# Kernel optimization log

Measured on AMD Instinct MI355X. Metric: run time of the kernel, lower is better.

The kernel has to match this reference:

```python
import jax, jax.numpy as jnp
import numpy as np

B = 64; SEQ = 512; PRED = 96; D = 321; HID = 2048
WIN = 64; STRIDE = WIN // 2; FT = WIN // 2 + 1
LOW = int(FT * 0.3); MID = int(FT * 0.4); HIGH = FT - LOW - MID  # 9, 13, 11
NW = SEQ // STRIDE + 1; EMBED = NW * WIN  # 17, 1088
EPS = 1e-5; SCALE = 0.02
LH = int(LOW * 2.0); MH = int(MID * 2.0); HH = int(HIGH * 2.0)  # 18, 26, 22


def _clayer(key, fan_in, fan_out):
    k1, k2, k3, k4 = jax.random.split(key, 4)
    return (jax.random.normal(k1, (fan_in, fan_out), jnp.float32) * SCALE,
            jax.random.normal(k2, (fan_in, fan_out), jnp.float32) * SCALE,
            jax.random.normal(k3, (fan_out,), jnp.float32) * SCALE,
            jax.random.normal(k4, (fan_out,), jnp.float32) * SCALE)


def setup_inputs() -> dict:
    key = jax.random.key(0)
    ks = jax.random.split(key, 12)
    inp = {}
    inp["x"] = jax.random.normal(ks[0], (B, SEQ, D), jnp.float32)
    inp["x_mark_enc"] = jax.random.normal(ks[1], (B, SEQ, 4), jnp.float32)
    inp["x_dec"] = jax.random.normal(ks[2], (B, PRED, D), jnp.float32)
    inp["x_mark_dec"] = jax.random.normal(ks[3], (B, PRED, 4), jnp.float32)
    n = jnp.arange(WIN, dtype=jnp.float32)
    inp["window"] = 0.5 * (1.0 - jnp.cos(2.0 * jnp.pi * n / WIN))  # torch.hann_window (periodic)
    inp["revin_w"] = jnp.ones((D,), jnp.float32)
    inp["revin_b"] = jnp.zeros((D,), jnp.float32)
    # low band filter: 3 complex layers LOW->LH->LH->LOW
    for i, (fi, fo) in enumerate([(LOW, LH), (LH, LH), (LH, LOW)]):
        wr, wi, br, bi = _clayer(jax.random.fold_in(ks[4], i), fi, fo)
        inp[f"low{i}_wr"], inp[f"low{i}_wi"], inp[f"low{i}_br"], inp[f"low{i}_bi"] = wr, wi, br, bi
    # mid band filter: 2 complex layers MID->MH->MID
    for i, (fi, fo) in enumerate([(MID, MH), (MH, MID)]):
        wr, wi, br, bi = _clayer(jax.random.fold_in(ks[5], i), fi, fo)
        inp[f"mid{i}_wr"], inp[f"mid{i}_wi"], inp[f"mid{i}_br"], inp[f"mid{i}_bi"] = wr, wi, br, bi
    # high band filter: 1 complex layer HIGH->HIGH
    wr, wi, br, bi = _clayer(ks[6], HIGH, HIGH)
    inp["high0_wr"], inp["high0_wi"], inp["high0_br"], inp["high0_bi"] = wr, wi, br, bi
    inp["fc1_w"] = jax.random.normal(ks[7], (EMBED, HID), jnp.float32) * SCALE
    inp["fc1_b"] = jnp.zeros((HID,), jnp.float32)
    inp["fc2_w"] = jax.random.normal(ks[8], (HID, PRED), jnp.float32) * SCALE
    inp["fc2_b"] = jnp.zeros((PRED,), jnp.float32)
    return inp


def _clin(z, wr, wi, br, bi):
    return z @ (wr + 1j * wi) + (br + 1j * bi)


def _cact(z):
    return jax.nn.leaky_relu(z.real) + 1j * jax.nn.leaky_relu(z.imag)


def reference(x, x_mark_enc, x_dec, x_mark_dec, window, revin_w, revin_b,
              low0_wr, low0_wi, low0_br, low0_bi,
              low1_wr, low1_wi, low1_br, low1_bi,
              low2_wr, low2_wi, low2_br, low2_bi,
              mid0_wr, mid0_wi, mid0_br, mid0_bi,
              mid1_wr, mid1_wi, mid1_br, mid1_bi,
              high0_wr, high0_wi, high0_br, high0_bi,
              fc1_w, fc1_b, fc2_w, fc2_b):
    # RevIN norm over time dim
    mean = jnp.mean(x, axis=1, keepdims=True)
    std = jnp.sqrt(jnp.var(x, axis=1, keepdims=True) + EPS)
    xn = (x - mean) / std * revin_w + revin_b
    xc = jnp.transpose(xn, (0, 2, 1))                      # [B, D, L]
    xp = jnp.pad(xc, ((0, 0), (0, 0), (STRIDE, STRIDE)))
    # batched window extraction (replaces python loop over windows)
    idx = jnp.arange(NW)[:, None] * STRIDE + jnp.arange(WIN)[None, :]
    seg = xp[:, :, idx]
    w = window / jnp.linalg.norm(window)
    xf = jnp.fft.rfft(seg * w, axis=-1)                    # [B, D, NW, FT] complex
    low = xf[..., :LOW]
    mid = xf[..., LOW:LOW + MID]
    high = xf[..., LOW + MID:]
    low = _clin(_cact(_clin(_cact(_clin(low, low0_wr, low0_wi, low0_br, low0_bi)),
                            low1_wr, low1_wi, low1_br, low1_bi)),
                low2_wr, low2_wi, low2_br, low2_bi)
    mid = _clin(_cact(_clin(mid, mid0_wr, mid0_wi, mid0_br, mid0_bi)),
                mid1_wr, mid1_wi, mid1_br, mid1_bi)
    high = _clin(high, high0_wr, high0_wi, high0_br, high0_bi)
    xfil = jnp.concatenate([low, mid, high], axis=-1)      # [B, D, NW, FT]
    xt = jnp.fft.irfft(xfil, n=WIN, axis=-1)
    emb = xt.reshape(x.shape[0], D, EMBED)
    h = jax.nn.leaky_relu(emb @ fc1_w + fc1_b)
    y = h @ fc2_w + fc2_b                                  # [B, D, PRED]
    y = jnp.transpose(y, (0, 2, 1))                        # [B, PRED, D]
    # RevIN denorm
    y = (y - revin_b) / (revin_w + EPS * EPS) * std + mean
    return y
```

## Files before the change

### kernel.cpp

```cpp
#include <hip/hip_runtime.h>

typedef unsigned short u16;
typedef unsigned int   u32;
typedef __attribute__((ext_vector_type(4))) float  fvec4;
typedef __attribute__((ext_vector_type(8))) __bf16 bvec8;

#define NB    64
#define SEQL  512
#define DCH   321
#define BDTOT (NB * DCH)
#define NWIN  17
#define PREDL 96
#define MWTOT (BDTOT * NWIN)
#define KPAD  1152

__device__ __forceinline__ u16 f2bf(float f) {
    union { float f; u32 u; } v; v.f = f;
    u32 r = v.u + 0x7FFFu + ((v.u >> 16) & 1u);
    return (u16)(r >> 16);
}
__device__ __forceinline__ float lrelu(float v) { return v > 0.f ? v : 0.01f * v; }

__device__ __forceinline__ void gld16(const u16* g, u16* l) {
    __builtin_amdgcn_global_load_lds((const __attribute__((address_space(1))) void*)g,
                                     (__attribute__((address_space(3))) void*)l, 16, 0, 0);
}

__global__ __launch_bounds__(256) void stats_kernel(const float* __restrict__ x,
                                                    float* __restrict__ mean,
                                                    float* __restrict__ rstd,
                                                    float* __restrict__ stdv) {
    __shared__ float ls[2][4][64];
    int i = threadIdx.x & 63;
    int j = threadIdx.x >> 6;
    int bd = blockIdx.x * 64 + i;
    int b = bd / DCH, d = bd - b * DCH;
    float s = 0.f, ss = 0.f;
    for (int t = j; t < SEQL; t += 4) {
        float v = x[((size_t)b * SEQL + t) * DCH + d];
        s += v; ss += v * v;
    }
    ls[0][j][i] = s; ls[1][j][i] = ss;
    __syncthreads();
    if (j == 0) {
        s  = ls[0][0][i] + ls[0][1][i] + ls[0][2][i] + ls[0][3][i];
        ss = ls[1][0][i] + ls[1][1][i] + ls[1][2][i] + ls[1][3][i];
        float m   = s * (1.f / SEQL);
        float var = ss * (1.f / SEQL) - m * m;
        float st  = sqrtf(var + 1e-5f);
        mean[bd] = m; rstd[bd] = 1.f / st; stdv[bd] = st;
    }
}

__global__ __launch_bounds__(256) void norm_transpose(const float* __restrict__ x,
                                                      const float* __restrict__ mean,
                                                      const float* __restrict__ rstd,
                                                      const float* __restrict__ rw,
                                                      const float* __restrict__ rb,
                                                      u16* __restrict__ xnT) {
    __shared__ float tile[64][65];
    int d0 = blockIdx.x * 64, s0 = blockIdx.y * 64, b = blockIdx.z;
    for (int e = threadIdx.x; e < 4096; e += 256) {
        int sr = e >> 6, dc = e & 63;
        int d = d0 + dc;
        tile[sr][dc] = (d < DCH) ? x[((size_t)b * SEQL + s0 + sr) * DCH + d] : 0.f;
    }
    __syncthreads();
    for (int e = threadIdx.x; e < 4096; e += 256) {
        int dr = e >> 6, sc = e & 63;
        int d = d0 + dr;
        if (d < DCH) {
            int bd = b * DCH + d;
            float v = (tile[sc][dr] - mean[bd]) * rstd[bd] * rw[d] + rb[d];
            xnT[(size_t)bd * 576 + 32 + s0 + sc] = f2bf(v);
        }
    }
}

__global__ __launch_bounds__(256) void pad_zero(u16* __restrict__ xnT) {
    int idx = blockIdx.x * 256 + threadIdx.x;
    if (idx < BDTOT * 64) {
        int bd = idx >> 6, q = idx & 63;
        int off = q < 32 ? q : 512 + q;
        xnT[(size_t)bd * 576 + off] = 0;
    }
}

__global__ __launch_bounds__(256) void pad_emb(u16* __restrict__ EMB) {
    int idx = blockIdx.x * 256 + threadIdx.x;
    if (idx < BDTOT * 8) {
        int bd = idx >> 3, o = (idx & 7) * 8;
        fvec4 z = {0.f, 0.f, 0.f, 0.f};
        *(fvec4*)&EMB[(size_t)bd * KPAD + 1088 + o] = z;
    }
}

__global__ __launch_bounds__(256) void precompute_kernel(
    const float* __restrict__ window,
    const float* __restrict__ l0wr, const float* __restrict__ l0wi,
    const float* __restrict__ l0br, const float* __restrict__ l0bi,
    const float* __restrict__ l1wr, const float* __restrict__ l1wi,
    const float* __restrict__ l1br, const float* __restrict__ l1bi,
    const float* __restrict__ l2wr, const float* __restrict__ l2wi,
    const float* __restrict__ l2br, const float* __restrict__ l2bi,
    const float* __restrict__ m0wr, const float* __restrict__ m0wi,
    const float* __restrict__ m0br, const float* __restrict__ m0bi,
    const float* __restrict__ m1wr, const float* __restrict__ m1wi,
    const float* __restrict__ m1br, const float* __restrict__ m1bi,
    const float* __restrict__ h0wr, const float* __restrict__ h0wi,
    const float* __restrict__ h0br, const float* __restrict__ h0bi,
    u16* __restrict__ A1t, u16* __restrict__ W1t, u16* __restrict__ B2t,
    float* __restrict__ bias1, float* __restrict__ bias2, float* __restrict__ biast)
{
    int idx = blockIdx.x * 256 + threadIdx.x;
    float nrm = 0.f;
    for (int i = 0; i < 64; ++i) nrm += window[i] * window[i];
    float inv = 1.0f / sqrtf(nrm);
    const float STEP = 6.283185307179586f / 64.f;
    auto Cc = [&](int n, int k) { return  window[n] * inv * cosf(STEP * (float)((k * n) & 63)); };
    auto Ss = [&](int n, int k) { return -window[n] * inv * sinf(STEP * (float)((k * n) & 63)); };
    auto aRe = [&](int k, int n) {
        float sc = (k == 0 || k == 32) ? (1.f / 64.f) : (2.f / 64.f);
        return sc * cosf(STEP * (float)((k * n) & 63));
    };
    auto aIm = [&](int k, int n) {
        if (k == 0 || k == 32) return 0.f;
        return -(2.f / 64.f) * sinf(STEP * (float)((k * n) & 63));
    };
    if (idx < 16384) {
        int j = idx >> 6, n = idx & 63;
        float v = 0.f;
        if (j < 18)                    { for (int k = 0; k < 9;  ++k) v += Cc(n,k)   *l0wr[k*18+j]      - Ss(n,k)   *l0wi[k*18+j]; }
        else if (j < 36)               { int jj=j-18; for (int k = 0; k < 9;  ++k) v += Cc(n,k)   *l0wi[k*18+jj] + Ss(n,k)   *l0wr[k*18+jj]; }
        else if (j >= 64  && j < 90)   { int jj=j-64; for (int k = 0; k < 13; ++k) v += Cc(n,9+k) *m0wr[k*26+jj] - Ss(n,9+k) *m0wi[k*26+jj]; }
        else if (j >= 90  && j < 116)  { int jj=j-90; for (int k = 0; k < 13; ++k) v += Cc(n,9+k) *m0wi[k*26+jj] + Ss(n,9+k) *m0wr[k*26+jj]; }
        else if (j >= 128 && j < 139)  { int jj=j-128;for (int k = 0; k < 11; ++k) v += Cc(n,22+k)*h0wr[k*11+jj] - Ss(n,22+k)*h0wi[k*11+jj]; }
        else if (j >= 139 && j < 150)  { int jj=j-139;for (int k = 0; k < 11; ++k) v += Cc(n,22+k)*h0wi[k*11+jj] + Ss(n,22+k)*h0wr[k*11+jj]; }
        A1t[idx] = f2bf(v);
    } else if (idx < 24576) {
        int t = idx - 16384; int j = t >> 6, k = t & 63;
        float v = 0.f;
        if (j < 18)      { if (k < 18) v = l1wr[k*18+j];        else if (k < 36) v = -l1wi[(k-18)*18+j]; }
        else if (j < 36) { int jj=j-18; if (k < 18) v = l1wi[k*18+jj]; else if (k < 36) v =  l1wr[(k-18)*18+jj]; }
        W1t[t] = f2bf(v);
    } else if (idx < 49152) {
        int t = idx - 24576; int n = t / 192, c = t - n * 192;
        float v = 0.f;
        if (n < 64) {
            if (c < 18)                  { for (int m = 0; m < 9;  ++m) v +=  l2wr[c*9+m]     *aRe(m,n)   + l2wi[c*9+m]     *aIm(m,n); }
            else if (c < 36)             { int cc=c-18; for (int m = 0; m < 9;  ++m) v += -l2wi[cc*9+m]   *aRe(m,n)   + l2wr[cc*9+m]   *aIm(m,n); }
            else if (c >= 64 && c < 90)  { int cc=c-64; for (int m = 0; m < 13; ++m) v +=  m1wr[cc*13+m]  *aRe(9+m,n) + m1wi[cc*13+m]  *aIm(9+m,n); }
            else if (c >= 90 && c < 116) { int cc=c-90; for (int m = 0; m < 13; ++m) v += -m1wi[cc*13+m]  *aRe(9+m,n) + m1wr[cc*13+m]  *aIm(9+m,n); }
            else if (c >= 128 && c < 139){ v = aRe(22 + (c-128), n); }
            else if (c >= 139 && c < 150){ v = aIm(22 + (c-139), n); }
        }
        B2t[t] = f2bf(v);
    } else if (idx < 49344) {
        int c = idx - 49152;
        float v = 0.f;
        if (c < 18) v = l0br[c];
        else if (c < 36) v = l0bi[c-18];
        else if (c >= 64 && c < 90) v = m0br[c-64];
        else if (c >= 90 && c < 116) v = m0bi[c-90];
        bias1[c] = v;
    } else if (idx < 49472) {
        int c = idx - 49344;
        float v = 0.f;
        if (c < 18) v = l1br[c]; else if (c < 36) v = l1bi[c-18];
        bias2[c] = v;
    } else if (idx < 49536) {
        int n = idx - 49472;
        float v = 0.f;
        for (int k = 0; k <= 32; ++k) {
            float br = (k < 9) ? l2br[k] : (k < 22 ? m1br[k-9] : h0br[k-22]);
            float bi = (k < 9) ? l2bi[k] : (k < 22 ? m1bi[k-9] : h0bi[k-22]);
            v += aRe(k, n) * br + aIm(k, n) * bi;
        }
        biast[n] = v;
    }
}

__global__ __launch_bounds__(256) void wtrans(const float* __restrict__ W, u16* __restrict__ Wt,
                                              int R, int C, int Cpad, int ldw) {
    __shared__ float t[32][33];
    int c0 = blockIdx.x * 32, r0 = blockIdx.y * 32;
    for (int e = threadIdx.x; e < 1024; e += 256) {
        int rr = e >> 5, cc = e & 31;
        int rg = r0 + rr, cg = c0 + cc;
        t[rr][cc] = (rg < R && cg < C) ? W[(size_t)rg * C + cg] : 0.f;
    }
    __syncthreads();
    for (int e = threadIdx.x; e < 1024; e += 256) {
        int cr = e >> 5, rc = e & 31;
        int cg = c0 + cr, rg = r0 + rc;
        if (cg < Cpad && rg < ldw) Wt[(size_t)cg * ldw + rg] = f2bf(t[rc][cr]);
    }
}

__global__ __launch_bounds__(256) void spectral_fused(
    const u16* __restrict__ xnT, const u16* __restrict__ A1t,
    const u16* __restrict__ W1t, const u16* __restrict__ B2t,
    const float* __restrict__ bias1, const float* __restrict__ bias2,
    const float* __restrict__ biast, u16* __restrict__ EMB)
{
    __shared__ u16 XB[64 * 72];
    __shared__ u16 ACT[64 * 208];
    const int tid  = threadIdx.x;
    const int lane = tid & 63;
    const int wn   = tid >> 6;
    const int r0   = blockIdx.x * 64;

    {
        int rr = tid >> 2;
        int cc = (tid & 3) * 16;
        u32 gr = (u32)(r0 + rr);
        u32 bd = gr / 17u, nw = gr - bd * 17u;
        const u16* src = xnT + (size_t)bd * 576 + nw * 32 + cc;
        *(bvec8*)&XB[rr * 72 + cc]     = *(const bvec8*)(src);
        *(bvec8*)&XB[rr * 72 + cc + 8] = *(const bvec8*)(src + 8);
    }
    __syncthreads();

    fvec4 acc1[4][3] = {};
#pragma unroll
    for (int kk = 0; kk < 2; ++kk) {
        int ko = kk * 32 + ((lane >> 4) << 3);
        bvec8 af[4], bf[3];
#pragma unroll
        for (int m = 0; m < 4; ++m)
            af[m] = *(const bvec8*)&XB[(m * 16 + (lane & 15)) * 72 + ko];
#pragma unroll
        for (int n = 0; n < 3; ++n)
            bf[n] = *(const bvec8*)(A1t + (size_t)(wn * 48 + n * 16 + (lane & 15)) * 64 + ko);
#pragma unroll
        for (int m = 0; m < 4; ++m)
#pragma unroll
            for (int n = 0; n < 3; ++n)
                acc1[m][n] = __builtin_amdgcn_mfma_f32_16x16x32_bf16(af[m], bf[n], acc1[m][n], 0, 0, 0);
    }
#pragma unroll
    for (int n = 0; n < 3; ++n) {
        int col = wn * 48 + n * 16 + (lane & 15);
        float bs = bias1[col];
#pragma unroll
        for (int m = 0; m < 4; ++m)
#pragma unroll
            for (int q = 0; q < 4; ++q) {
                int row = m * 16 + ((lane >> 4) << 2) + q;
                float v = acc1[m][n][q] + bs;
                if (col < 128) v = lrelu(v);
                ACT[row * 208 + col] = f2bf(v);
            }
    }
    __syncthreads();

    fvec4 acc2[4] = {};
#pragma unroll
    for (int kk = 0; kk < 2; ++kk) {
        int ko = kk * 32 + ((lane >> 4) << 3);
        bvec8 bf = *(const bvec8*)(W1t + (size_t)(wn * 16 + (lane & 15)) * 64 + ko);
#pragma unroll
        for (int m = 0; m < 4; ++m) {
            bvec8 af = *(const bvec8*)&ACT[(m * 16 + (lane & 15)) * 208 + ko];
            acc2[m] = __builtin_amdgcn_mfma_f32_16x16x32_bf16(af, bf, acc2[m], 0, 0, 0);
        }
    }
    __syncthreads();
    {
        int col = wn * 16 + (lane & 15);
        float bs = bias2[col];
#pragma unroll
        for (int m = 0; m < 4; ++m)
#pragma unroll
            for (int q = 0; q < 4; ++q) {
                int row = m * 16 + ((lane >> 4) << 2) + q;
                ACT[row * 208 + col] = f2bf(lrelu(acc2[m][q] + bs));
            }
    }
    __syncthreads();

    fvec4 acc3[4] = {};
#pragma unroll
    for (int kk = 0; kk < 6; ++kk) {
        int ko = kk * 32 + ((lane >> 4) << 3);
        bvec8 bf = *(const bvec8*)(B2t + (size_t)(wn * 16 + (lane & 15)) * 192 + ko);
#pragma unroll
        for (int m = 0; m < 4; ++m) {
            bvec8 af = *(const bvec8*)&ACT[(m * 16 + (lane & 15)) * 208 + ko];
            acc3[m] = __builtin_amdgcn_mfma_f32_16x16x32_bf16(af, bf, acc3[m], 0, 0, 0);
        }
    }
    {
        int col = wn * 16 + (lane & 15);
        float bs = biast[col];
#pragma unroll
        for (int m = 0; m < 4; ++m)
#pragma unroll
            for (int q = 0; q < 4; ++q) {
                int row = m * 16 + ((lane >> 4) << 2) + q;
                int wr = r0 + row;
                int bd2 = wr / 17, nw2 = wr - bd2 * 17;
                EMB[(size_t)bd2 * KPAD + nw2 * 64 + col] = f2bf(acc3[m][q] + bs);
            }
    }
}

template <int SWZ>
__global__ __launch_bounds__(512, 2) void gemm256_m201(
    const u16* __restrict__ A, const u16* __restrict__ Bt,
    const float* __restrict__ bias, u16* __restrict__ C,
    int Mloc, int K, int ldc, long long a_off, int nwg)
{
    extern __shared__ u16 lds[];
    const int tid  = threadIdx.x;
    const int lane = tid & 63;
    const int l15  = lane & 15;
    const int hi   = lane >> 4;
    const int wid  = tid >> 6;
    const int wm   = wid >> 2;
    const int wn   = wid & 3;
    int wg;
    if (SWZ) {
        int bid = blockIdx.x;
        int q = nwg >> 3, r = nwg & 7, xcd = bid & 7, off = bid >> 3;
        wg = (xcd < r) ? (xcd * (q + 1) + off) : (r * (q + 1) + (xcd - r) * q + off);
    } else wg = blockIdx.x;
    const int mt = wg >> 3;
    const int nt = wg & 7;
    const int bm0 = mt * 256, bn0 = nt * 256;

    const u16* sbase[4][2];
#pragma unroll
    for (int u = 0; u < 4; ++u) {
#pragma unroll
        for (int j = 0; j < 2; ++j) {
            int idx = j * 512 + tid;
            if ((u & 1) == 0) {
                int row = (u >> 1) * 128 + (idx >> 3);
                int kc = ((idx & 7) ^ (row & 7)) << 3;
                int rl = bm0 + row; if (rl > Mloc - 1) rl = Mloc - 1;
                sbase[u][j] = A + (size_t)(a_off + rl) * K + kc;
            } else {
                int row = idx >> 2;
                int kc = (u >> 1) * 32 + (((idx & 3) ^ ((row >> 1) & 3)) << 3);
                sbase[u][j] = Bt + (size_t)(bn0 + row) * K + kc;
            }
        }
    }
    auto stage_unit = [&](int bufb, int tg, int u) {
        int base = ((u & 1) == 0) ? ((u >> 1) * 8192) : (16384 + (u >> 1) * 8192);
        u16* dstb = lds + bufb * 32768 + base;
#pragma unroll
        for (int j = 0; j < 2; ++j) {
            int idx = j * 512 + tid;
            gld16(sbase[u][j] + ((size_t)tg << 6), dstb + idx * 8);
        }
    };

    fvec4 acc[8][4] = {};
    const int NT = K >> 6;

    stage_unit(0, 0, 0); stage_unit(0, 0, 1); stage_unit(0, 0, 2); stage_unit(0, 0, 3);
    asm volatile("s_waitcnt vmcnt(4)");
    __builtin_amdgcn_s_barrier();

    for (int t = 0; t < NT; ++t) {
        const int cur = t & 1;
        const u16* Ab = lds + cur * 32768;
        const u16* Bb = Ab + 16384;
        const bool nl = (t < NT - 1);
        bvec8 bfr[4];
#pragma unroll
        for (int p = 0; p < 4; ++p) {
            const int kk = p >> 1, mh = p & 1;
            bvec8 af[4];
            if (mh == 0) {
#pragma unroll
                for (int n = 0; n < 4; ++n) {
                    int r = wn * 64 + n * 16 + l15;
                    int ch = hi ^ ((r >> 1) & 3);
                    bfr[n] = *(const bvec8*)&Bb[kk * 8192 + r * 32 + ch * 8];
                }
            }
#pragma unroll
            for (int mm = 0; mm < 4; ++mm) {
                int r = mh * 128 + wm * 64 + mm * 16 + l15;
                int ch = (kk * 4 + hi) ^ (r & 7);
                af[mm] = *(const bvec8*)&Ab[r * 64 + ch * 8];
            }
            if (nl) stage_unit(cur ^ 1, t + 1, p);
            __builtin_amdgcn_s_barrier();
            asm volatile("s_waitcnt lgkmcnt(0)");
            __builtin_amdgcn_s_setprio(1);
#pragma unroll
            for (int mm = 0; mm < 4; ++mm)
#pragma unroll
                for (int n = 0; n < 4; ++n)
                    acc[mh * 4 + mm][n] = __builtin_amdgcn_mfma_f32_16x16x32_bf16(
                        af[mm], bfr[n], acc[mh * 4 + mm][n], 0, 0, 0);
            __builtin_amdgcn_s_setprio(0);
            if (p == 0) {
                if (nl) asm volatile("s_waitcnt vmcnt(4)");
                else    asm volatile("s_waitcnt vmcnt(2)");
            } else if (p == 1) {
                if (nl) asm volatile("s_waitcnt vmcnt(4)");
                else    asm volatile("s_waitcnt vmcnt(0)");
            } else if (p == 3) {
                if (nl) asm volatile("s_waitcnt vmcnt(4)");
            }
            __builtin_amdgcn_s_barrier();
        }
    }

#pragma unroll
    for (int m = 0; m < 8; ++m) {
        int mh = m >> 2, mm = m & 3;
        int rl0 = bm0 + mh * 128 + wm * 64 + mm * 16 + hi * 4;
#pragma unroll
        for (int n = 0; n < 4; ++n) {
            int col = bn0 + wn * 64 + n * 16 + l15;
            float bs = bias[col];
#pragma unroll
            for (int q = 0; q < 4; ++q) {
                int rl = rl0 + q;
                if (rl < Mloc)
                    C[(size_t)rl * (size_t)ldc + col] = f2bf(lrelu(acc[m][n][q] + bs));
            }
        }
    }
}

__global__ __launch_bounds__(256) void gemm_bt_splitk(
    const u16* __restrict__ A, const u16* __restrict__ Bt,
    void* __restrict__ Cp, int Mloc, int N, int K, int lda, int ldc,
    long long c_off, int klen, long long pstride)
{
    const int tid  = threadIdx.x;
    const int lane = tid & 63;
    const int wm   = (tid >> 7) & 1;
    const int wn   = (tid >> 6) & 1;
    const int mt = blockIdx.y;
    int k0 = blockIdx.x * klen;
    int k1 = (k0 + klen > K) ? K : k0 + klen;
    const int bn0 = 0;
    const int bm0 = mt * 128;
    __shared__ u16 Als[128 * 64];
    __shared__ u16 Bls[128 * 64];
    fvec4 acc[4][4] = {};

    for (int kt = k0; kt < k1; kt += 64) {
#pragma unroll
        for (int i = 0; i < 4; ++i) {
            int idx = i * 256 + tid;
            int r  = idx >> 3;
            int kc = (idx & 7) << 3;
            int rl = bm0 + r; if (rl > Mloc - 1) rl = Mloc - 1;
            gld16(A + (size_t)rl * lda + kt + kc, &Als[idx * 8]);
            gld16(Bt + (size_t)(bn0 + r) * K + kt + kc, &Bls[idx * 8]);
        }
        __syncthreads();
#pragma unroll
        for (int kk = 0; kk < 2; ++kk) {
            int ko = kk * 32 + ((lane >> 4) << 3);
            bvec8 af[4], bfr[4];
#pragma unroll
            for (int m = 0; m < 4; ++m)
                af[m] = *(const bvec8*)&Als[(wm * 64 + m * 16 + (lane & 15)) * 64 + ko];
#pragma unroll
            for (int n = 0; n < 4; ++n)
                bfr[n] = *(const bvec8*)&Bls[(wn * 64 + n * 16 + (lane & 15)) * 64 + ko];
#pragma unroll
            for (int m = 0; m < 4; ++m)
#pragma unroll
                for (int n = 0; n < 4; ++n)
                    acc[m][n] = __builtin_amdgcn_mfma_f32_16x16x32_bf16(af[m], bfr[n], acc[m][n], 0, 0, 0);
        }
        __syncthreads();
    }

#pragma unroll
    for (int m = 0; m < 4; ++m) {
        int rbase = bm0 + wm * 64 + m * 16 + ((lane >> 4) << 2);
#pragma unroll
        for (int n = 0; n < 4; ++n) {
            int col = bn0 + wn * 64 + n * 16 + (lane & 15);
            if (col < N) {
#pragma unroll
                for (int q = 0; q < 4; ++q) {
                    int rl = rbase + q;
                    if (rl < Mloc) {
                        float* yp = (float*)Cp + (size_t)blockIdx.x * pstride;
                        yp[(size_t)(c_off + rl) * ldc + col] = acc[m][n][q];
                    }
                }
            }
        }
    }
}

__global__ __launch_bounds__(256) void final_denorm(const float* __restrict__ YP,
                                                    const float* __restrict__ fc2b,
                                                    const float* __restrict__ mean,
                                                    const float* __restrict__ stdv,
                                                    const float* __restrict__ rw,
                                                    const float* __restrict__ rb,
                                                    float* __restrict__ out) {
    const long long PART = (long long)BDTOT * PREDL;
    __shared__ float t[32][33];
    int d0 = blockIdx.x * 32, p0 = blockIdx.y * 32, b = blockIdx.z;
    for (int e = threadIdx.x; e < 1024; e += 256) {
        int di = e >> 5, pj = e & 31;
        int d = d0 + di, p = p0 + pj;
        if (d < DCH && p < PREDL) {
            size_t off = ((size_t)b * DCH + d) * PREDL + p;
            t[di][pj] = YP[off] + YP[off + PART] + YP[off + 2 * PART] + fc2b[p];
        } else t[di][pj] = 0.f;
    }
    __syncthreads();
    for (int e = threadIdx.x; e < 1024; e += 256) {
        int pi = e >> 5, dj = e & 31;
        int d = d0 + dj, p = p0 + pi;
        if (d < DCH && p < PREDL) {
            int bd = b * DCH + d;
            float v = (t[dj][pi] - rb[d]) / (rw[d] + 1e-10f) * stdv[bd] + mean[bd];
            out[((size_t)b * PREDL + p) * DCH + d] = v;
        }
    }
}

extern "C" void kernel_launch(void* const* d_in, const int* in_sizes, int n_in,
                              void* d_out, int out_size, void* d_ws, size_t ws_size,
                              hipStream_t stream) {
    const float* x      = (const float*)d_in[0];
    const float* window = (const float*)d_in[4];
    const float* rw     = (const float*)d_in[5];
    const float* rb     = (const float*)d_in[6];
    const float* l0wr = (const float*)d_in[7],  *l0wi = (const float*)d_in[8];
    const float* l0br = (const float*)d_in[9],  *l0bi = (const float*)d_in[10];
    const float* l1wr = (const float*)d_in[11], *l1wi = (const float*)d_in[12];
    const float* l1br = (const float*)d_in[13], *l1bi = (const float*)d_in[14];
    const float* l2wr = (const float*)d_in[15], *l2wi = (const float*)d_in[16];
    const float* l2br = (const float*)d_in[17], *l2bi = (const float*)d_in[18];
    const float* m0wr = (const float*)d_in[19], *m0wi = (const float*)d_in[20];
    const float* m0br = (const float*)d_in[21], *m0bi = (const float*)d_in[22];
    const float* m1wr = (const float*)d_in[23], *m1wi = (const float*)d_in[24];
    const float* m1br = (const float*)d_in[25], *m1bi = (const float*)d_in[26];
    const float* h0wr = (const float*)d_in[27], *h0wi = (const float*)d_in[28];
    const float* h0br = (const float*)d_in[29], *h0bi = (const float*)d_in[30];
    const float* fc1w = (const float*)d_in[31];
    const float* fc1b = (const float*)d_in[32];
    const float* fc2w = (const float*)d_in[33];
    const float* fc2b = (const float*)d_in[34];

    char* p = (char*)d_ws;
    auto alloc = [&](size_t n) { char* r = p; p += (n + 255) & ~(size_t)255; return r; };
    float* mean  = (float*)alloc(BDTOT * 4);
    float* rstd  = (float*)alloc(BDTOT * 4);
    float* stdv  = (float*)alloc(BDTOT * 4);
    float* bias1 = (float*)alloc(192 * 4);
    float* bias2 = (float*)alloc(128 * 4);
    float* biast = (float*)alloc(64 * 4);
    u16* A1t   = (u16*)alloc(256 * 64 * 2);
    u16* W1t   = (u16*)alloc(128 * 64 * 2);
    u16* B2t   = (u16*)alloc(128 * 192 * 2);
    u16* fc1wT = (u16*)alloc((size_t)2048 * KPAD * 2);
    u16* fc2wT = (u16*)alloc((size_t)128 * 2048 * 2);
    u16* xnT   = (u16*)alloc((size_t)BDTOT * 576 * 2);
    float* YP  = (float*)xnT;
    u16* EMB   = (u16*)alloc((size_t)BDTOT * KPAD * 2);

    size_t fixed_end = (size_t)(p - (char*)d_ws);
    int CH = 16;
    const int chs[5] = {1, 2, 4, 8, 16};
    for (int ci = 0; ci < 5; ++ci) {
        int c = chs[ci];
        size_t hbuf = (size_t)(BDTOT / c) * 2048 * 2;
        if (fixed_end + hbuf <= ws_size) { CH = c; break; }
    }
    int bd_c = BDTOT / CH;
    u16* Hbuf = (u16*)p;

    hipFuncSetAttribute(reinterpret_cast<const void*>(&gemm256_m201<1>),
                        hipFuncAttributeMaxDynamicSharedMemorySize, 131072);

    dim3 blk(256);
    stats_kernel<<<BDTOT / 64, blk, 0, stream>>>(x, mean, rstd, stdv);
    norm_transpose<<<dim3(6, 8, NB), blk, 0, stream>>>(x, mean, rstd, rw, rb, xnT);
    pad_zero<<<(BDTOT * 64 + 255) / 256, blk, 0, stream>>>(xnT);
    precompute_kernel<<<194, blk, 0, stream>>>(window,
        l0wr, l0wi, l0br, l0bi, l1wr, l1wi, l1br, l1bi, l2wr, l2wi, l2br, l2bi,
        m0wr, m0wi, m0br, m0bi, m1wr, m1wi, m1br, m1bi, h0wr, h0wi, h0br, h0bi,
        A1t, W1t, B2t, bias1, bias2, biast);
    wtrans<<<dim3(64, 36), blk, 0, stream>>>(fc1w, fc1wT, 1088, 2048, 2048, KPAD);
    wtrans<<<dim3(4, 64),  blk, 0, stream>>>(fc2w, fc2wT, 2048, 96, 128, 2048);

    spectral_fused<<<MWTOT / 64, blk, 0, stream>>>(xnT, A1t, W1t, B2t, bias1, bias2, biast, EMB);
    pad_emb<<<(BDTOT * 8 + 255) / 256, blk, 0, stream>>>(EMB);

    const long long PART = (long long)BDTOT * PREDL;
    for (int c = 0; c < CH; ++c) {
        long long boff = (long long)c * bd_c;
        int gm = (bd_c + 255) / 256;
        int nwg = 8 * gm;
        gemm256_m201<1><<<dim3(nwg), dim3(512), 131072, stream>>>(EMB, fc1wT, fc1b, Hbuf,
            bd_c, KPAD, 2048, boff, nwg);
        gemm_bt_splitk<<<dim3(3, (bd_c + 127) / 128), blk, 0, stream>>>(Hbuf, fc2wT, YP,
            bd_c, 96, 2048, 2048, 96, boff, 704, PART);
    }
    final_denorm<<<dim3(11, 3, NB), blk, 0, stream>>>(YP, fc2b, mean, stdv, rw, rb, (float*)d_out);
}
```

Measured before the change: 320.6 us.

## Fuse fc2 GEMM into fc1 GEMM epilogue with per-N-tile partial outputs

Each fc1 workgroup now keeps its 256x256 leaky-ReLU output tile in LDS (XOR-swizzled) and multiplies it straight away by the matching 256-row slice of fc2 weights, writing fp32 partial predictions into 8 per-column-tile buffers. The later denorm kernel sums these 8 partials. This removes the bf16 hidden-activation round trip through global memory, the separate split-K fc2 kernel and the chunked launch loop. It also merges the two padding kernels into one launch. In exchange it writes 8x partial outputs, reads fc2 weights from global inside each workgroup, and adds more epilogue work to the main GEMM.

New measurement: 295.3 us. 7.9% less time.

```diff
diff --git a/kernel.cpp b/kernel.cpp
--- a/kernel.cpp
+++ b/kernel.cpp
@@ -77,19 +77,15 @@
     }
 }
 
-__global__ __launch_bounds__(256) void pad_zero(u16* __restrict__ xnT) {
+__global__ __launch_bounds__(256) void pads(u16* __restrict__ xnT, u16* __restrict__ EMB) {
     int idx = blockIdx.x * 256 + threadIdx.x;
     if (idx < BDTOT * 64) {
         int bd = idx >> 6, q = idx & 63;
         int off = q < 32 ? q : 512 + q;
         xnT[(size_t)bd * 576 + off] = 0;
-    }
-}
-
-__global__ __launch_bounds__(256) void pad_emb(u16* __restrict__ EMB) {
-    int idx = blockIdx.x * 256 + threadIdx.x;
-    if (idx < BDTOT * 8) {
-        int bd = idx >> 3, o = (idx & 7) * 8;
+    } else if (idx < BDTOT * 64 + BDTOT * 8) {
+        int t = idx - BDTOT * 64;
+        int bd = t >> 3, o = (t & 7) * 8;
         fvec4 z = {0.f, 0.f, 0.f, 0.f};
         *(fvec4*)&EMB[(size_t)bd * KPAD + 1088 + o] = z;
     }
@@ -306,10 +302,11 @@
 }
 
 template <int SWZ>
-__global__ __launch_bounds__(512, 2) void gemm256_m201(
+__global__ __launch_bounds__(512, 2) void gemm_fused(
     const u16* __restrict__ A, const u16* __restrict__ Bt,
-    const float* __restrict__ bias, u16* __restrict__ C,
-    int Mloc, int K, int ldc, long long a_off, int nwg)
+    const float* __restrict__ bias, const u16* __restrict__ W2t,
+    float* __restrict__ YP,
+    int Mloc, int K, long long a_off, int nwg)
 {
     extern __shared__ u16 lds[];
     const int tid  = threadIdx.x;
@@ -415,84 +412,47 @@
 #pragma unroll
     for (int m = 0; m < 8; ++m) {
         int mh = m >> 2, mm = m & 3;
-        int rl0 = bm0 + mh * 128 + wm * 64 + mm * 16 + hi * 4;
+        int row0 = mh * 128 + wm * 64 + mm * 16 + hi * 4;
 #pragma unroll
         for (int n = 0; n < 4; ++n) {
-            int col = bn0 + wn * 64 + n * 16 + l15;
-            float bs = bias[col];
+            int col = wn * 64 + n * 16 + l15;
+            float bs = bias[bn0 + col];
 #pragma unroll
             for (int q = 0; q < 4; ++q) {
-                int rl = rl0 + q;
-                if (rl < Mloc)
-                    C[(size_t)rl * (size_t)ldc + col] = f2bf(lrelu(acc[m][n][q] + bs));
-            }
-        }
-    }
-}
-
-__global__ __launch_bounds__(256) void gemm_bt_splitk(
-    const u16* __restrict__ A, const u16* __restrict__ Bt,
-    void* __restrict__ Cp, int Mloc, int N, int K, int lda, int ldc,
-    long long c_off, int klen, long long pstride)
-{
-    const int tid  = threadIdx.x;
-    const int lane = tid & 63;
-    const int wm   = (tid >> 7) & 1;
-    const int wn   = (tid >> 6) & 1;
-    const int mt = blockIdx.y;
-    int k0 = blockIdx.x * klen;
-    int k1 = (k0 + klen > K) ? K : k0 + klen;
-    const int bn0 = 0;
-    const int bm0 = mt * 128;
-    __shared__ u16 Als[128 * 64];
-    __shared__ u16 Bls[128 * 64];
-    fvec4 acc[4][4] = {};
-
-    for (int kt = k0; kt < k1; kt += 64) {
-#pragma unroll
-        for (int i = 0; i < 4; ++i) {
-            int idx = i * 256 + tid;
-            int r  = idx >> 3;
-            int kc = (idx & 7) << 3;
-            int rl = bm0 + r; if (rl > Mloc - 1) rl = Mloc - 1;
-            gld16(A + (size_t)rl * lda + kt + kc, &Als[idx * 8]);
-            gld16(Bt + (size_t)(bn0 + r) * K + kt + kc, &Bls[idx * 8]);
-        }
-        __syncthreads();
-#pragma unroll
-        for (int kk = 0; kk < 2; ++kk) {
-            int ko = kk * 32 + ((lane >> 4) << 3);
-            bvec8 af[4], bfr[4];
-#pragma unroll
-            for (int m = 0; m < 4; ++m)
-                af[m] = *(const bvec8*)&Als[(wm * 64 + m * 16 + (lane & 15)) * 64 + ko];
-#pragma unroll
-            for (int n = 0; n < 4; ++n)
-                bfr[n] = *(const bvec8*)&Bls[(wn * 64 + n * 16 + (lane & 15)) * 64 + ko];
-#pragma unroll
-            for (int m = 0; m < 4; ++m)
-#pragma unroll
-                for (int n = 0; n < 4; ++n)
-                    acc[m][n] = __builtin_amdgcn_mfma_f32_16x16x32_bf16(af[m], bfr[n], acc[m][n], 0, 0, 0);
-        }
-        __syncthreads();
-    }
-
-#pragma unroll
-    for (int m = 0; m < 4; ++m) {
-        int rbase = bm0 + wm * 64 + m * 16 + ((lane >> 4) << 2);
-#pragma unroll
-        for (int n = 0; n < 4; ++n) {
-            int col = bn0 + wn * 64 + n * 16 + (lane & 15);
-            if (col < N) {
-#pragma unroll
-                for (int q = 0; q < 4; ++q) {
-                    int rl = rbase + q;
-                    if (rl < Mloc) {
-                        float* yp = (float*)Cp + (size_t)blockIdx.x * pstride;
-                        yp[(size_t)(c_off + rl) * ldc + col] = acc[m][n][q];
-                    }
-                }
+                int r = row0 + q;
+                lds[r * 256 + (((col >> 3) ^ (r & 7)) << 3) + (col & 7)] =
+                    f2bf(lrelu(acc[m][n][q] + bs));
+            }
+        }
+    }
+    __syncthreads();
+
+    fvec4 acc2[2][6] = {};
+    const int wr0 = wid * 32;
+#pragma unroll
+    for (int ks = 0; ks < 8; ++ks) {
+        bvec8 bw[6];
+#pragma unroll
+        for (int cf = 0; cf < 6; ++cf)
+            bw[cf] = *(const bvec8*)(W2t + (size_t)(cf * 16 + l15) * 2048 + bn0 + ks * 32 + hi * 8);
+#pragma unroll
+        for (int rf = 0; rf < 2; ++rf) {
+            int r = wr0 + rf * 16 + l15;
+            bvec8 ah = *(const bvec8*)&lds[r * 256 + (((ks * 4 + hi) ^ (r & 7)) << 3)];
+#pragma unroll
+            for (int cf = 0; cf < 6; ++cf)
+                acc2[rf][cf] = __builtin_amdgcn_mfma_f32_16x16x32_bf16(ah, bw[cf], acc2[rf][cf], 0, 0, 0);
+        }
+    }
+    float* yp = YP + (size_t)nt * ((size_t)BDTOT * PREDL);
+#pragma unroll
+    for (int rf = 0; rf < 2; ++rf) {
+#pragma unroll
+        for (int cf = 0; cf < 6; ++cf) {
+#pragma unroll
+            for (int q = 0; q < 4; ++q) {
+                int r = bm0 + wr0 + rf * 16 + hi * 4 + q;
+                if (r < Mloc) yp[(size_t)r * PREDL + cf * 16 + l15] = acc2[rf][cf][q];
             }
         }
     }
@@ -505,7 +465,7 @@
                                                     const float* __restrict__ rw,
                                                     const float* __restrict__ rb,
                                                     float* __restrict__ out) {
-    const long long PART = (long long)BDTOT * PREDL;
+    const size_t PART = (size_t)BDTOT * PREDL;
     __shared__ float t[32][33];
     int d0 = blockIdx.x * 32, p0 = blockIdx.y * 32, b = blockIdx.z;
     for (int e = threadIdx.x; e < 1024; e += 256) {
@@ -513,7 +473,10 @@
         int d = d0 + di, p = p0 + pj;
         if (d < DCH && p < PREDL) {
             size_t off = ((size_t)b * DCH + d) * PREDL + p;
-            t[di][pj] = YP[off] + YP[off + PART] + YP[off + 2 * PART] + fc2b[p];
+            float s = fc2b[p];
+#pragma unroll
+            for (int i = 0; i < 8; ++i) s += YP[off + (size_t)i * PART];
+            t[di][pj] = s;
         } else t[di][pj] = 0.f;
     }
     __syncthreads();
@@ -566,27 +529,16 @@
     u16* fc1wT = (u16*)alloc((size_t)2048 * KPAD * 2);
     u16* fc2wT = (u16*)alloc((size_t)128 * 2048 * 2);
     u16* xnT   = (u16*)alloc((size_t)BDTOT * 576 * 2);
-    float* YP  = (float*)xnT;
     u16* EMB   = (u16*)alloc((size_t)BDTOT * KPAD * 2);
-
-    size_t fixed_end = (size_t)(p - (char*)d_ws);
-    int CH = 16;
-    const int chs[5] = {1, 2, 4, 8, 16};
-    for (int ci = 0; ci < 5; ++ci) {
-        int c = chs[ci];
-        size_t hbuf = (size_t)(BDTOT / c) * 2048 * 2;
-        if (fixed_end + hbuf <= ws_size) { CH = c; break; }
-    }
-    int bd_c = BDTOT / CH;
-    u16* Hbuf = (u16*)p;
-
-    hipFuncSetAttribute(reinterpret_cast<const void*>(&gemm256_m201<1>),
+    float* YP  = (float*)alloc((size_t)8 * BDTOT * PREDL * 4);
+
+    hipFuncSetAttribute(reinterpret_cast<const void*>(&gemm_fused<1>),
                         hipFuncAttributeMaxDynamicSharedMemorySize, 131072);
 
     dim3 blk(256);
     stats_kernel<<<BDTOT / 64, blk, 0, stream>>>(x, mean, rstd, stdv);
     norm_transpose<<<dim3(6, 8, NB), blk, 0, stream>>>(x, mean, rstd, rw, rb, xnT);
-    pad_zero<<<(BDTOT * 64 + 255) / 256, blk, 0, stream>>>(xnT);
+    pads<<<(BDTOT * 72 + 255) / 256, blk, 0, stream>>>(xnT, EMB);
     precompute_kernel<<<194, blk, 0, stream>>>(window,
         l0wr, l0wi, l0br, l0bi, l1wr, l1wi, l1br, l1bi, l2wr, l2wi, l2br, l2bi,
         m0wr, m0wi, m0br, m0bi, m1wr, m1wi, m1br, m1bi, h0wr, h0wi, h0br, h0bi,
@@ -595,17 +547,12 @@
     wtrans<<<dim3(4, 64),  blk, 0, stream>>>(fc2w, fc2wT, 2048, 96, 128, 2048);
 
     spectral_fused<<<MWTOT / 64, blk, 0, stream>>>(xnT, A1t, W1t, B2t, bias1, bias2, biast, EMB);
-    pad_emb<<<(BDTOT * 8 + 255) / 256, blk, 0, stream>>>(EMB);
-
-    const long long PART = (long long)BDTOT * PREDL;
-    for (int c = 0; c < CH; ++c) {
-        long long boff = (long long)c * bd_c;
-        int gm = (bd_c + 255) / 256;
+
+    {
+        int gm = (BDTOT + 255) / 256;
         int nwg = 8 * gm;
-        gemm256_m201<1><<<dim3(nwg), dim3(512), 131072, stream>>>(EMB, fc1wT, fc1b, Hbuf,
-            bd_c, KPAD, 2048, boff, nwg);
-        gemm_bt_splitk<<<dim3(3, (bd_c + 127) / 128), blk, 0, stream>>>(Hbuf, fc2wT, YP,
-            bd_c, 96, 2048, 2048, 96, boff, 704, PART);
+        gemm_fused<1><<<dim3(nwg), dim3(512), 131072, stream>>>(EMB, fc1wT, fc1b, fc2wT, YP,
+            BDTOT, KPAD, 0, nwg);
     }
     final_denorm<<<dim3(11, 3, NB), blk, 0, stream>>>(YP, fc2b, mean, stdv, rw, rb, (float*)d_out);
 }
```
